# Optimization experiments

Measured on AMD Instinct MI355X. Metric: run time of the kernel, lower is better.

Reference implementation:

```python
import jax, jax.numpy as jnp
import numpy as np

N, F_IN, R, H, U, B, E = 20000, 256, 8, 4, 64, 4, 320000
NEG_SLOPE = 0.2  # torch F.leaky_relu default is 0.01, but GAT/RGAT uses 0.2; source uses F.leaky_relu -> 0.01
LRELU_SLOPE = 0.01


def setup_inputs() -> dict:
    key = jax.random.key(0)
    ks = jax.random.split(key, 8)
    x = jax.random.normal(ks[0], (N, F_IN), dtype=jnp.float32)
    basis = jax.random.normal(ks[1], (B, F_IN, U), dtype=jnp.float32) * 0.05
    coeff = jax.random.normal(ks[2], (R * H, B), dtype=jnp.float32)
    attn_q = jax.random.normal(ks[3], (R, H, U), dtype=jnp.float32) * 0.1
    attn_k = jax.random.normal(ks[4], (R, H, U), dtype=jnp.float32) * 0.1
    src = jax.random.randint(ks[5], (E,), 0, N, dtype=jnp.int32)
    dst = jax.random.randint(ks[6], (E,), 0, N, dtype=jnp.int32)
    rel = jax.random.randint(ks[7], (E,), 0, R, dtype=jnp.int32)
    return {"x": x, "basis": basis, "coeff": coeff, "attn_q": attn_q,
            "attn_k": attn_k, "src": src, "dst": dst, "rel": rel}


def reference(x, basis, coeff, attn_q, attn_k, src, dst, rel):
    n = x.shape[0]
    # Basis-decomposed relational kernels: W_{r,h} = sum_b c_{(r,h),b} W'_b
    W = jnp.einsum("cb,bfu->cfu", coeff, basis).reshape(R, H, F_IN, U)
    # Relation/head-specific projections: [N, R, H, U]
    xp = jnp.einsum("nf,rhfu->nrhu", x, W)
    # GAT-style 'sum' attention, attention_units=1: scalar query/key per (node, r, h)
    q = jnp.einsum("nrhu,rhu->nrh", xp, attn_q)  # [N, R, H]
    k = jnp.einsum("nrhu,rhu->nrh", xp, attn_k)  # [N, R, H]
    # Per-edge logits, gathered along sparse support: [E, H]
    logit = jax.nn.leaky_relu(q[src, rel] + k[dst, rel], negative_slope=LRELU_SLOPE)
    # ARGAT: segment softmax per destination node across all relations/edges
    m = jax.ops.segment_max(logit, dst, num_segments=n)        # [N, H]
    m = jnp.where(jnp.isfinite(m), m, 0.0)
    ex = jnp.exp(logit - m[dst])                               # [E, H]
    denom = jax.ops.segment_sum(ex, dst, num_segments=n)       # [N, H]
    alpha = ex / jnp.maximum(denom[dst], 1e-16)                # [E, H]
    # Weighted scatter-aggregation of messages: [N, H, U]
    msg = xp[src, rel] * alpha[:, :, None]                     # [E, H, U]
    out = jax.ops.segment_sum(msg, dst, num_segments=n)
    # head_aggregation='mean', activation=None, use_bias=False
    return out.mean(axis=1)  # [N, U]
```

## Files before the change

### kernel.cpp

```cpp
#include <hip/hip_runtime.h>
#include <hip/hip_bf16.h>
#include <math.h>

#define F_IN    256
#define R_REL   8
#define H_HEADS 4
#define U_DIM   64
#define B_BASES 4
#define C_TOT   (R_REL * H_HEADS)
#define LRELU   0.01f
#define SLOT_CAP 64

typedef __attribute__((ext_vector_type(8))) short short8;
typedef __attribute__((ext_vector_type(4))) float f32x4;

__device__ __forceinline__ unsigned short f2bf(float f) {
    unsigned int u = __float_as_uint(f);
    u = (u + 0x7FFF + ((u >> 16) & 1)) >> 16;
    return (unsigned short)u;
}
__device__ __forceinline__ float bf2f_lo(unsigned int v) { return __uint_as_float(v << 16); }
__device__ __forceinline__ float bf2f_hi(unsigned int v) { return __uint_as_float(v & 0xFFFF0000u); }

__global__ __launch_bounds__(256) void prep_all(const float* __restrict__ x,
                                                unsigned short* __restrict__ xb,
                                                int total4,
                                                int* __restrict__ counts,
                                                int n_nodes,
                                                const float* __restrict__ basis,
                                                const float* __restrict__ coeff,
                                                const float* __restrict__ attn_q,
                                                const float* __restrict__ attn_k,
                                                unsigned short* __restrict__ Wt,
                                                int n_cast_blocks) {
    if (blockIdx.x < (unsigned)n_cast_blocks) {
        int i = blockIdx.x * 256 + threadIdx.x;
        if (i < n_nodes) counts[i] = 0;
        if (i >= total4) return;
        float4 v = *(const float4*)&x[(size_t)i * 4];
        ushort4 o;
        o.x = f2bf(v.x); o.y = f2bf(v.y); o.z = f2bf(v.z); o.w = f2bf(v.w);
        *(ushort4*)&xb[(size_t)i * 4] = o;
        return;
    }

    __shared__ float aq[64], ak[64];
    int c = blockIdx.x - n_cast_blocks;
    int f = threadIdx.x;
    if (f < 64) {
        aq[f] = attn_q[c * 64 + f];
        ak[f] = attn_k[c * 64 + f];
    }
    __syncthreads();

    #pragma unroll
    for (int j = 0; j < 8; ++j) {
        int nn = c * 8 + j;
        int b = nn & 3, u = nn >> 2;
        Wt[(size_t)nn * 256 + f] = f2bf(basis[(size_t)b * (F_IN * U_DIM) + (size_t)f * U_DIM + u]);
    }

    float sq = 0.f, sk = 0.f;
    #pragma unroll
    for (int b = 0; b < B_BASES; ++b) {
        float cb = coeff[c * 4 + b];
        const float* bp = basis + (size_t)b * (F_IN * U_DIM) + (size_t)f * U_DIM;
        float dq = 0.f, dk = 0.f;
        #pragma unroll
        for (int u = 0; u < 64; ++u) {
            float v = bp[u];
            dq += v * aq[u];
            dk += v * ak[u];
        }
        sq += cb * dq;
        sk += cb * dk;
    }
    Wt[(size_t)(256 + c) * 256 + f] = f2bf(sq);
    Wt[(size_t)(288 + c) * 256 + f] = f2bf(sk);
}

__global__ __launch_bounds__(256) void gemm_fused(const unsigned short* __restrict__ xb,
                                                  const unsigned short* __restrict__ Wt,
                                                  unsigned short* __restrict__ zb,
                                                  float* __restrict__ qk,
                                                  const int* __restrict__ src,
                                                  const int* __restrict__ dst,
                                                  const int* __restrict__ rel,
                                                  int* __restrict__ counts,
                                                  unsigned int* __restrict__ slots,
                                                  int nrows, int E) {
    __shared__ unsigned short Al[128 * 72];
    __shared__ unsigned short Bl[128 * 72];

    const int tid  = threadIdx.x;
    const int wave = tid >> 6;
    const int lane = tid & 63;
    const int wr   = wave >> 1;
    const int wc   = wave & 1;
    const int m0   = blockIdx.x * 128;
    const int bb   = blockIdx.y;
    const int l15  = lane & 15;
    const int quad = lane >> 4;

    if (bb < 2) {
        f32x4 acc[4][4];
        #pragma unroll
        for (int t = 0; t < 4; ++t)
            #pragma unroll
            for (int s = 0; s < 4; ++s)
                acc[t][s] = (f32x4){0.f, 0.f, 0.f, 0.f};

        for (int k0 = 0; k0 < 256; k0 += 64) {
            #pragma unroll
            for (int p = 0; p < 4; ++p) {
                int idx = p * 256 + tid;
                int row = idx >> 3;
                int cg  = idx & 7;
                int gr  = m0 + row;
                uint4 v = make_uint4(0, 0, 0, 0);
                if (gr < nrows) v = *(const uint4*)&xb[(size_t)gr * 256 + k0 + cg * 8];
                *(uint4*)&Al[row * 72 + cg * 8] = v;
            }
            #pragma unroll
            for (int p = 0; p < 4; ++p) {
                int idx = p * 256 + tid;
                int row = idx >> 3;
                int cg  = idx & 7;
                uint4 v = *(const uint4*)&Wt[(size_t)(bb * 128 + row) * 256 + k0 + cg * 8];
                *(uint4*)&Bl[row * 72 + cg * 8] = v;
            }
            __syncthreads();

            #pragma unroll
            for (int ks = 0; ks < 64; ks += 32) {
                short8 wf[4];
                #pragma unroll
                for (int s = 0; s < 4; ++s)
                    wf[s] = *(short8*)&Bl[(wc * 64 + s * 16 + l15) * 72 + ks + quad * 8];
                #pragma unroll
                for (int t = 0; t < 4; ++t) {
                    short8 xf = *(short8*)&Al[(wr * 64 + t * 16 + l15) * 72 + ks + quad * 8];
                    #pragma unroll
                    for (int s = 0; s < 4; ++s)
                        acc[t][s] = __builtin_amdgcn_mfma_f32_16x16x32_bf16(wf[s], xf, acc[t][s], 0, 0, 0);
                }
            }
            __syncthreads();
        }

        #pragma unroll
        for (int t = 0; t < 4; ++t) {
            int m = m0 + wr * 64 + t * 16 + l15;
            if (m < nrows) {
                #pragma unroll
                for (int s = 0; s < 4; ++s) {
                    int c = bb * 128 + wc * 64 + s * 16 + quad * 4;
                    ushort4 o;
                    o.x = f2bf(acc[t][s][0]);
                    o.y = f2bf(acc[t][s][1]);
                    o.z = f2bf(acc[t][s][2]);
                    o.w = f2bf(acc[t][s][3]);
                    *(ushort4*)&zb[(size_t)m * 256 + c] = o;
                }
            }
        }
    } else {
        f32x4 acc[4][2];
        #pragma unroll
        for (int t = 0; t < 4; ++t)
            #pragma unroll
            for (int s = 0; s < 2; ++s)
                acc[t][s] = (f32x4){0.f, 0.f, 0.f, 0.f};

        for (int k0 = 0; k0 < 256; k0 += 64) {
            #pragma unroll
            for (int p = 0; p < 4; ++p) {
                int idx = p * 256 + tid;
                int row = idx >> 3;
                int cg  = idx & 7;
                int gr  = m0 + row;
                uint4 v = make_uint4(0, 0, 0, 0);
                if (gr < nrows) v = *(const uint4*)&xb[(size_t)gr * 256 + k0 + cg * 8];
                *(uint4*)&Al[row * 72 + cg * 8] = v;
            }
            #pragma unroll
            for (int p = 0; p < 2; ++p) {
                int idx = p * 256 + tid;
                int row = idx >> 3;
                int cg  = idx & 7;
                uint4 v = *(const uint4*)&Wt[(size_t)(256 + row) * 256 + k0 + cg * 8];
                *(uint4*)&Bl[row * 72 + cg * 8] = v;
            }
            __syncthreads();

            #pragma unroll
            for (int ks = 0; ks < 64; ks += 32) {
                short8 wf[2];
                #pragma unroll
                for (int s = 0; s < 2; ++s)
                    wf[s] = *(short8*)&Bl[(wc * 32 + s * 16 + l15) * 72 + ks + quad * 8];
                #pragma unroll
                for (int t = 0; t < 4; ++t) {
                    short8 xf = *(short8*)&Al[(wr * 64 + t * 16 + l15) * 72 + ks + quad * 8];
                    #pragma unroll
                    for (int s = 0; s < 2; ++s)
                        acc[t][s] = __builtin_amdgcn_mfma_f32_16x16x32_bf16(wf[s], xf, acc[t][s], 0, 0, 0);
                }
            }
            __syncthreads();
        }

        #pragma unroll
        for (int t = 0; t < 4; ++t) {
            int m = m0 + wr * 64 + t * 16 + l15;
            if (m < nrows) {
                #pragma unroll
                for (int s = 0; s < 2; ++s) {
                    int c = wc * 32 + s * 16 + quad * 4;
                    float4 o = make_float4(acc[t][s][0], acc[t][s][1],
                                           acc[t][s][2], acc[t][s][3]);
                    *(float4*)&qk[(size_t)m * 64 + c] = o;
                }
            }
        }

        int stride = gridDim.x * 256;
        int base = blockIdx.x * 256 + tid;
        for (int i = base; i < E; i += stride) {
            int d = dst[i];
            int pos = atomicAdd(&counts[d], 1);
            if (pos < SLOT_CAP)
                slots[(size_t)d * SLOT_CAP + pos] = (unsigned)src[i] | ((unsigned)rel[i] << 20);
        }
    }
}

__global__ __launch_bounds__(256) void agg_kernel(const unsigned short* __restrict__ zb,
                                                  const float* __restrict__ qk,
                                                  const float* __restrict__ coeff,
                                                  const unsigned int* __restrict__ slots,
                                                  const int* __restrict__ counts,
                                                  float* __restrict__ out,
                                                  int n_nodes) {
    __shared__ float cf[128];
    __shared__ float4 gsh[4][64];
    __shared__ int    ssh[4][64];
    if (threadIdx.x < 128) cf[threadIdx.x] = coeff[threadIdx.x];
    __syncthreads();

    int wv   = threadIdx.x >> 6;
    int n    = blockIdx.x * 4 + wv;
    int lane = threadIdx.x & 63;
    if (n >= n_nodes) return;

    int cnt = counts[n];
    if (cnt > SLOT_CAP) cnt = SLOT_CAP;
    const unsigned int* sl = slots + (size_t)n * SLOT_CAP;

    float e0 = 0.f, e1 = 0.f, e2 = 0.f, e3 = 0.f;
    int s_edge = 0, r_edge = 0;
    if (lane < cnt) {
        unsigned p = sl[lane];
        s_edge = (int)(p & 0xFFFFFu);
        r_edge = (int)(p >> 20);
        float4 q  = *(const float4*)&qk[(size_t)s_edge * 64 + r_edge * 4];
        float4 kv = *(const float4*)&qk[(size_t)n * 64 + 32 + r_edge * 4];
        float l0 = q.x + kv.x, l1 = q.y + kv.y, l2 = q.z + kv.z, l3 = q.w + kv.w;
        l0 = (l0 > 0.f) ? l0 : LRELU * l0;
        l1 = (l1 > 0.f) ? l1 : LRELU * l1;
        l2 = (l2 > 0.f) ? l2 : LRELU * l2;
        l3 = (l3 > 0.f) ? l3 : LRELU * l3;
        e0 = __expf(l0); e1 = __expf(l1); e2 = __expf(l2); e3 = __expf(l3);
    }
    float d0 = e0, d1 = e1, d2 = e2, d3 = e3;
    #pragma unroll
    for (int off = 32; off; off >>= 1) {
        d0 += __shfl_xor(d0, off);
        d1 += __shfl_xor(d1, off);
        d2 += __shfl_xor(d2, off);
        d3 += __shfl_xor(d3, off);
    }
    if (lane < cnt) {
        float a0 = e0 * ((d0 > 0.f) ? 0.25f / d0 : 0.f);
        float a1 = e1 * ((d1 > 0.f) ? 0.25f / d1 : 0.f);
        float a2 = e2 * ((d2 > 0.f) ? 0.25f / d2 : 0.f);
        float a3 = e3 * ((d3 > 0.f) ? 0.25f / d3 : 0.f);
        const float* c0 = &cf[(r_edge * 4 + 0) * 4];
        const float* c1 = &cf[(r_edge * 4 + 1) * 4];
        const float* c2 = &cf[(r_edge * 4 + 2) * 4];
        const float* c3 = &cf[(r_edge * 4 + 3) * 4];
        float4 g4;
        g4.x = a0 * c0[0] + a1 * c1[0] + a2 * c2[0] + a3 * c3[0];
        g4.y = a0 * c0[1] + a1 * c1[1] + a2 * c2[1] + a3 * c3[1];
        g4.z = a0 * c0[2] + a1 * c1[2] + a2 * c2[2] + a3 * c3[2];
        g4.w = a0 * c0[3] + a1 * c1[3] + a2 * c2[3] + a3 * c3[3];
        gsh[wv][lane] = g4;
        ssh[wv][lane] = s_edge;
    }

    int es = lane >> 3;
    int g  = lane & 7;
    float acc[4][2];
    #pragma unroll
    for (int v = 0; v < 4; ++v) { acc[v][0] = 0.f; acc[v][1] = 0.f; }

    for (int base = 0; base < cnt; base += 8) {
        int i = base + es;
        if (i < cnt) {
            float4 g4 = gsh[wv][i];
            int s = ssh[wv][i];
            const unsigned short* zr = zb + (size_t)s * 256 + g * 8;
            #pragma unroll
            for (int v = 0; v < 4; ++v) {
                uint4 z4 = *(const uint4*)(zr + v * 64);
                acc[v][0] += g4.x * bf2f_lo(z4.x) + g4.y * bf2f_hi(z4.x) +
                             g4.z * bf2f_lo(z4.y) + g4.w * bf2f_hi(z4.y);
                acc[v][1] += g4.x * bf2f_lo(z4.z) + g4.y * bf2f_hi(z4.z) +
                             g4.z * bf2f_lo(z4.w) + g4.w * bf2f_hi(z4.w);
            }
        }
    }

    #pragma unroll
    for (int v = 0; v < 4; ++v) {
        #pragma unroll
        for (int j = 0; j < 2; ++j) {
            acc[v][j] += __shfl_xor(acc[v][j], 8);
            acc[v][j] += __shfl_xor(acc[v][j], 16);
            acc[v][j] += __shfl_xor(acc[v][j], 32);
        }
    }
    if (es == 0) {
        #pragma unroll
        for (int v = 0; v < 4; ++v) {
            float2 o = make_float2(acc[v][0], acc[v][1]);
            *(float2*)&out[(size_t)n * 64 + v * 16 + g * 2] = o;
        }
    }
}

extern "C" void kernel_launch(void* const* d_in, const int* in_sizes, int n_in,
                              void* d_out, int out_size, void* d_ws, size_t ws_size,
                              hipStream_t stream) {
    const float* x      = (const float*)d_in[0];
    const float* basis  = (const float*)d_in[1];
    const float* coeff  = (const float*)d_in[2];
    const float* attn_q = (const float*)d_in[3];
    const float* attn_k = (const float*)d_in[4];
    const int*   src    = (const int*)d_in[5];
    const int*   dst    = (const int*)d_in[6];
    const int*   rel    = (const int*)d_in[7];
    float* out = (float*)d_out;

    const int n_nodes = in_sizes[0] / F_IN;
    const int E       = in_sizes[5];

    char* ws = (char*)d_ws;
    size_t off = 0;
    auto alloc = [&](size_t bytes) -> void* {
        void* p = ws + off;
        off += bytes;
        off = (off + 255) & ~(size_t)255;
        return p;
    };
    unsigned short* xb   = (unsigned short*)alloc((size_t)n_nodes * 256 * 2);
    unsigned short* Wt   = (unsigned short*)alloc((size_t)320 * 256 * 2);
    unsigned short* zb   = (unsigned short*)alloc((size_t)n_nodes * 256 * 2);
    float* qk            = (float*)alloc((size_t)n_nodes * 64 * 4);
    unsigned int* slots  = (unsigned int*)alloc((size_t)n_nodes * SLOT_CAP * 4);
    int* counts          = (int*)alloc((size_t)n_nodes * 4);

    const int total4 = n_nodes * 64;
    const int n_cast_blocks = (total4 + 255) / 256;

    prep_all<<<n_cast_blocks + C_TOT, 256, 0, stream>>>(
        x, xb, total4, counts, n_nodes, basis, coeff, attn_q, attn_k, Wt, n_cast_blocks);

    dim3 g2((n_nodes + 127) / 128, 3);
    gemm_fused<<<g2, 256, 0, stream>>>(xb, Wt, zb, qk, src, dst, rel, counts, slots,
                                       n_nodes, E);

    agg_kernel<<<(n_nodes + 3) / 4, 256, 0, stream>>>(zb, qk, coeff, slots, counts, out, n_nodes);
}
```

Baseline: 146.4 us.

## Split edge bucketing into separate grid row and transpose MFMA operand order

Moves the per-edge atomic bucketing of edges into slots out of the qk GEMM blocks and into a dedicated fourth row of the grid, so bucketing runs in parallel with the GEMM tiles instead of serially after the qk tile. It also swaps the MFMA operand order, which transposes the accumulator layout. The epilogue therefore now writes scalar elements, one column per lane, instead of packed ushort4/float4 row vectors. This adds more blocks but makes the output stores narrower and less coalesced per row.

```diff
diff --git a/kernel.cpp b/kernel.cpp
--- a/kernel.cpp
+++ b/kernel.cpp
@@ -79,16 +79,28 @@
     Wt[(size_t)(288 + c) * 256 + f] = f2bf(sk);
 }
 
-__global__ __launch_bounds__(256) void gemm_fused(const unsigned short* __restrict__ xb,
-                                                  const unsigned short* __restrict__ Wt,
-                                                  unsigned short* __restrict__ zb,
-                                                  float* __restrict__ qk,
-                                                  const int* __restrict__ src,
-                                                  const int* __restrict__ dst,
-                                                  const int* __restrict__ rel,
-                                                  int* __restrict__ counts,
-                                                  unsigned int* __restrict__ slots,
-                                                  int nrows, int E) {
+__global__ __launch_bounds__(256) void gemm_scatter(const unsigned short* __restrict__ xb,
+                                                    const unsigned short* __restrict__ Wt,
+                                                    unsigned short* __restrict__ zb,
+                                                    float* __restrict__ qk,
+                                                    const int* __restrict__ src,
+                                                    const int* __restrict__ dst,
+                                                    const int* __restrict__ rel,
+                                                    int* __restrict__ counts,
+                                                    unsigned int* __restrict__ slots,
+                                                    int nrows, int E) {
+    if (blockIdx.y == 3) {
+        int stride = gridDim.x * 256;
+        int base = blockIdx.x * 256 + threadIdx.x;
+        for (int i = base; i < E; i += stride) {
+            int d = dst[i];
+            int pos = atomicAdd(&counts[d], 1);
+            if (pos < SLOT_CAP)
+                slots[(size_t)d * SLOT_CAP + pos] = (unsigned)src[i] | ((unsigned)rel[i] << 20);
+        }
+        return;
+    }
+
     __shared__ unsigned short Al[128 * 72];
     __shared__ unsigned short Bl[128 * 72];
 
@@ -133,16 +145,16 @@
 
             #pragma unroll
             for (int ks = 0; ks < 64; ks += 32) {
-                short8 wf[4];
+                short8 bfr[4];
                 #pragma unroll
                 for (int s = 0; s < 4; ++s)
-                    wf[s] = *(short8*)&Bl[(wc * 64 + s * 16 + l15) * 72 + ks + quad * 8];
+                    bfr[s] = *(short8*)&Bl[(wc * 64 + s * 16 + l15) * 72 + ks + quad * 8];
                 #pragma unroll
                 for (int t = 0; t < 4; ++t) {
-                    short8 xf = *(short8*)&Al[(wr * 64 + t * 16 + l15) * 72 + ks + quad * 8];
+                    short8 afr = *(short8*)&Al[(wr * 64 + t * 16 + l15) * 72 + ks + quad * 8];
                     #pragma unroll
                     for (int s = 0; s < 4; ++s)
-                        acc[t][s] = __builtin_amdgcn_mfma_f32_16x16x32_bf16(wf[s], xf, acc[t][s], 0, 0, 0);
+                        acc[t][s] = __builtin_amdgcn_mfma_f32_16x16x32_bf16(afr, bfr[s], acc[t][s], 0, 0, 0);
                 }
             }
             __syncthreads();
@@ -150,17 +162,14 @@
 
         #pragma unroll
         for (int t = 0; t < 4; ++t) {
-            int m = m0 + wr * 64 + t * 16 + l15;
-            if (m < nrows) {
-                #pragma unroll
-                for (int s = 0; s < 4; ++s) {
-                    int c = bb * 128 + wc * 64 + s * 16 + quad * 4;
-                    ushort4 o;
-                    o.x = f2bf(acc[t][s][0]);
-                    o.y = f2bf(acc[t][s][1]);
-                    o.z = f2bf(acc[t][s][2]);
-                    o.w = f2bf(acc[t][s][3]);
-                    *(ushort4*)&zb[(size_t)m * 256 + c] = o;
+            #pragma unroll
+            for (int s = 0; s < 4; ++s) {
+                int c_local = bb * 128 + wc * 64 + s * 16 + l15;
+                #pragma unroll
+                for (int reg = 0; reg < 4; ++reg) {
+                    int m = m0 + wr * 64 + t * 16 + quad * 4 + reg;
+                    if (m < nrows)
+                        zb[(size_t)m * 256 + c_local] = f2bf(acc[t][s][reg]);
                 }
             }
         }
@@ -195,16 +204,16 @@
 
             #pragma unroll
             for (int ks = 0; ks < 64; ks += 32) {
-                short8 wf[2];
+                short8 bfr[2];
                 #pragma unroll
                 for (int s = 0; s < 2; ++s)
-                    wf[s] = *(short8*)&Bl[(wc * 32 + s * 16 + l15) * 72 + ks + quad * 8];
+                    bfr[s] = *(short8*)&Bl[(wc * 32 + s * 16 + l15) * 72 + ks + quad * 8];
                 #pragma unroll
                 for (int t = 0; t < 4; ++t) {
-                    short8 xf = *(short8*)&Al[(wr * 64 + t * 16 + l15) * 72 + ks + quad * 8];
+                    short8 afr = *(short8*)&Al[(wr * 64 + t * 16 + l15) * 72 + ks + quad * 8];
                     #pragma unroll
                     for (int s = 0; s < 2; ++s)
-                        acc[t][s] = __builtin_amdgcn_mfma_f32_16x16x32_bf16(wf[s], xf, acc[t][s], 0, 0, 0);
+                        acc[t][s] = __builtin_amdgcn_mfma_f32_16x16x32_bf16(afr, bfr[s], acc[t][s], 0, 0, 0);
                 }
             }
             __syncthreads();
@@ -212,25 +221,16 @@
 
         #pragma unroll
         for (int t = 0; t < 4; ++t) {
-            int m = m0 + wr * 64 + t * 16 + l15;
-            if (m < nrows) {
-                #pragma unroll
-                for (int s = 0; s < 2; ++s) {
-                    int c = wc * 32 + s * 16 + quad * 4;
-                    float4 o = make_float4(acc[t][s][0], acc[t][s][1],
-                                           acc[t][s][2], acc[t][s][3]);
-                    *(float4*)&qk[(size_t)m * 64 + c] = o;
+            #pragma unroll
+            for (int s = 0; s < 2; ++s) {
+                int c_local = wc * 32 + s * 16 + l15;
+                #pragma unroll
+                for (int reg = 0; reg < 4; ++reg) {
+                    int m = m0 + wr * 64 + t * 16 + quad * 4 + reg;
+                    if (m < nrows)
+                        qk[(size_t)m * 64 + c_local] = acc[t][s][reg];
                 }
             }
-        }
-
-        int stride = gridDim.x * 256;
-        int base = blockIdx.x * 256 + tid;
-        for (int i = base; i < E; i += stride) {
-            int d = dst[i];
-            int pos = atomicAdd(&counts[d], 1);
-            if (pos < SLOT_CAP)
-                slots[(size_t)d * SLOT_CAP + pos] = (unsigned)src[i] | ((unsigned)rel[i] << 20);
         }
     }
 }
@@ -376,9 +376,9 @@
     prep_all<<<n_cast_blocks + C_TOT, 256, 0, stream>>>(
         x, xb, total4, counts, n_nodes, basis, coeff, attn_q, attn_k, Wt, n_cast_blocks);
 
-    dim3 g2((n_nodes + 127) / 128, 3);
-    gemm_fused<<<g2, 256, 0, stream>>>(xb, Wt, zb, qk, src, dst, rel, counts, slots,
-                                       n_nodes, E);
+    dim3 g2((n_nodes + 127) / 128, 4);
+    gemm_scatter<<<g2, 256, 0, stream>>>(xb, Wt, zb, qk, src, dst, rel, counts, slots,
+                                         n_nodes, E);
 
     agg_kernel<<<(n_nodes + 3) / 4, 256, 0, stream>>>(zb, qk, coeff, slots, counts, out, n_nodes);
 }
```

Measured after the change: 142.6 us. -2.6%, faster.
